# Kernel optimization log

Hardware: AMD Instinct MI355X
Metric: run time of the kernel (lower is better)

Reference implementation:

```python
import jax, jax.numpy as jnp
import numpy as np

V, E, D_LAT, NC, L = 30000, 256, 256, 10, 4096
B = 8
D_IN = 2 * D_LAT   # mamba expand=2 -> 512
N_ST = 16          # d_state
DT_R = 16          # dt_rank = ceil(d_model/16)
D_CONV = 4


def conv1d(x, w, b, pad, groups=1):
    # x: [B,C,L], w: [O, C//groups, K] (torch layout)
    y = jax.lax.conv_general_dilated(x, w, (1,), [(pad[0], pad[1])],
                                     dimension_numbers=('NCH', 'OIH', 'NCH'),
                                     feature_group_count=groups)
    return y + b[None, :, None]


def setup_inputs() -> dict:
    key = jax.random.key(0)
    ks = jax.random.split(key, 12)
    nrm = lambda k, s, sc=0.02: (jax.random.normal(k, s) * sc).astype(jnp.float32)
    return {
        'tokens': jax.random.randint(ks[0], (B, L), 0, V),
        'emb': nrm(ks[1], (V, E)),
        'conv1_w': nrm(ks[2], (128, E, 5)), 'conv1_b': jnp.zeros((128,), jnp.float32),
        'conv2_w': nrm(ks[3], (D_LAT, 128, 3)), 'conv2_b': jnp.zeros((D_LAT,), jnp.float32),
        'in_proj_w': nrm(ks[4], (2 * D_IN, D_LAT)),
        'convdw_w': nrm(ks[5], (D_IN, 1, D_CONV), 0.2), 'convdw_b': jnp.zeros((D_IN,), jnp.float32),
        'x_proj_w': nrm(ks[6], (DT_R + 2 * N_ST, D_IN)),
        'dt_proj_w': nrm(ks[7], (D_IN, DT_R), 0.1),
        'dt_proj_b': jnp.full((D_IN,), -4.0, jnp.float32),  # softplus^-1 of small dt
        'A_log': jnp.broadcast_to(jnp.log(jnp.arange(1, N_ST + 1, dtype=jnp.float32)), (D_IN, N_ST)) + jnp.zeros((D_IN, N_ST), jnp.float32),
        'Dp': jnp.ones((D_IN,), jnp.float32),
        'out_proj_w': nrm(ks[8], (D_LAT, D_IN)),
        'fc_w': nrm(ks[9], (NC, D_LAT)), 'fc_b': jnp.zeros((NC,), jnp.float32),
    }


def mamba_block(u, in_proj_w, convdw_w, convdw_b, x_proj_w, dt_proj_w, dt_proj_b, A_log, Dp, out_proj_w):
    # u: [B, Lm, d_model]
    Bsz = u.shape[0]
    xz = u @ in_proj_w.T                              # [B,Lm,2*Din]
    x, z = jnp.split(xz, 2, axis=-1)
    # causal depthwise conv (torch pads both sides, slices [:L] == left-pad only)
    xc = conv1d(x.transpose(0, 2, 1), convdw_w, convdw_b, (D_CONV - 1, 0), groups=D_IN)
    x = jax.nn.silu(xc.transpose(0, 2, 1))            # [B,Lm,Din]
    dbc = x @ x_proj_w.T                              # [B,Lm,dt_rank+2N]
    dt, Bm, Cm = jnp.split(dbc, [DT_R, DT_R + N_ST], axis=-1)
    dt = jax.nn.softplus(dt @ dt_proj_w.T + dt_proj_b)  # [B,Lm,Din]
    A = -jnp.exp(A_log)                               # [Din,N]

    def step(h, inp):
        dt_t, B_t, C_t, x_t = inp                     # [B,Din],[B,N],[B,N],[B,Din]
        dA = jnp.exp(dt_t[..., None] * A)             # [B,Din,N]
        h = h * dA + (dt_t * x_t)[..., None] * B_t[:, None, :]
        y = jnp.einsum('bdn,bn->bd', h, C_t)
        return h, y

    h0 = jnp.zeros((Bsz, D_IN, N_ST), u.dtype)
    xs = (dt.transpose(1, 0, 2), Bm.transpose(1, 0, 2), Cm.transpose(1, 0, 2), x.transpose(1, 0, 2))
    _, ys = jax.lax.scan(step, h0, xs)                # [Lm,B,Din]
    y = ys.transpose(1, 0, 2) + x * Dp
    y = y * jax.nn.silu(z)
    return y @ out_proj_w.T                           # [B,Lm,d_model]


def reference(tokens, emb, conv1_w, conv1_b, conv2_w, conv2_b, in_proj_w, convdw_w, convdw_b,
              x_proj_w, dt_proj_w, dt_proj_b, A_log, Dp, out_proj_w, fc_w, fc_b):
    x = emb[tokens]                                   # [B,L,E]
    x = x.transpose(0, 2, 1)                          # [B,E,L]
    x = jax.nn.relu(conv1d(x, conv1_w, conv1_b, (2, 2)))
    b, c, l = x.shape
    x = x.reshape(b, c, l // 2, 2).max(-1)            # MaxPool1d(2)
    x = jax.nn.relu(conv1d(x, conv2_w, conv2_b, (1, 1)))
    x = x.transpose(0, 2, 1)                          # [B,L/2,latent]
    x = mamba_block(x, in_proj_w, convdw_w, convdw_b, x_proj_w, dt_proj_w, dt_proj_b, A_log, Dp, out_proj_w)
    x = x.mean(axis=1)                                # [B,latent]
    return x @ fc_w.T + fc_b                          # [B,num_classes]
```

## Files before the change

kernel.cpp:

```cpp
#include <hip/hip_runtime.h>
#include <hip/hip_bf16.h>

constexpr int Bn   = 8;
constexpr int L    = 4096;
constexpr int E    = 256;
constexpr int Lh   = 2048;
constexpr int C1n  = 128;
constexpr int Dlat = 256;
constexpr int Din  = 512;
constexpr int Nst  = 16;
constexpr int M2   = Bn * Lh;
constexpr int NCH  = 128;
constexpr int TC   = 16;

constexpr long o_wtx   = 0;
constexpr long o_wtdt  = o_wtx  + 512L*48;
constexpr long o_bf    = o_wtdt + 16L*512;
constexpr long o_xeb   = o_bf    + 524288/2;
constexpr long o_out1b = o_xeb   + (8L*4100*256)/2;
constexpr long o_ub    = o_out1b + (8L*2050*128)/2;
constexpr long o_xz    = o_ub    + (16384L*256)/2;
constexpr long o_xbuf  = o_xz    + 16384L*1024;
constexpr long o_dbc   = o_xbuf  + 16384L*512;
constexpr long o_hend  = o_dbc   + 16384L*48;
constexpr long o_P     = o_hend  + 8L*512*NCH*16;
constexpr long o_S     = o_P     + 8L*512*NCH*16;
constexpr long o_ym    = o_S     + 8L*512*NCH*16;
constexpr long o_yp    = o_ym    + 8L*512;

typedef __attribute__((ext_vector_type(8))) short bf8_t;
typedef __attribute__((ext_vector_type(4))) float f4_t;

__device__ inline short f2bf(float f) {
    unsigned int u = __float_as_uint(f);
    unsigned int r = (u + 0x7FFFu + ((u >> 16) & 1u)) >> 16;
    return (short)r;
}

__global__ void k_prep(const float* __restrict__ w1, const float* __restrict__ w2,
                       const float* __restrict__ win, const float* __restrict__ xw,
                       const float* __restrict__ dtw, float* __restrict__ ws) {
    int idx = blockIdx.x * 256 + threadIdx.x;
    if (idx < 24576) {
        int n_ = idx % 48; int k = idx / 48;
        ws[o_wtx + idx] = xw[n_*512 + k];
    } else if (idx < 32768) {
        int j = idx - 24576;
        int n_ = j & 511; int k = j >> 9;
        ws[o_wtdt + j] = dtw[n_*16 + k];
    } else if (idx < 557056) {
        int j = idx - 32768;
        short* wsS = (short*)(ws + o_bf);
        if (j < 163840) {
            int n_ = j / 1280; int r = j - n_*1280; int s = r >> 8; int c = r & 255;
            wsS[j] = f2bf(w1[(n_*256 + c)*5 + s]);
        } else if (j < 262144) {
            int jj = j - 163840;
            int n_ = jj / 384; int r = jj - n_*384; int s = r >> 7; int c = r & 127;
            wsS[j] = f2bf(w2[(n_*128 + c)*3 + s]);
        } else {
            int jj = j - 262144;
            int n_ = jj >> 8; int k = jj & 255;
            wsS[j] = f2bf(win[n_*256 + k]);
        }
    }
}

__global__ void k_embed(const int* __restrict__ tok, const float* __restrict__ emb,
                        short* __restrict__ xeb) {
    int idx = blockIdx.x * 256 + threadIdx.x;
    int r = idx >> 5;
    int c8 = (idx & 31) << 3;
    int b = r / 4100; int tr = r - b*4100;
    bf8_t v = {0,0,0,0,0,0,0,0};
    if (tr >= 2 && tr < 4098) {
        int t = tok[b*4096 + tr - 2];
        const float* e = emb + (long)t*256 + c8;
        #pragma unroll
        for (int i = 0; i < 8; ++i) v[i] = f2bf(e[i]);
    }
    *(bf8_t*)&xeb[(long)r*256 + c8] = v;
}

__global__ void k_zpad(short* __restrict__ out1b) {
    int i = threadIdx.x;
    for (int j = i; j < 2048; j += 256) {
        int b = j >> 8; int rsel = (j >> 7) & 1; int c = j & 127;
        long row = (long)b*2050 + (rsel ? 2049 : 0);
        out1b[row*128 + c] = 0;
    }
}

template<int SHIFTS, int TPS, int EPI>
__global__ __launch_bounds__(256) void k_mgemm(const short* __restrict__ A, int ars, long batchA,
                                               const short* __restrict__ Bt, int ktot,
                                               const float* __restrict__ bias,
                                               short* __restrict__ outB, float* __restrict__ outF,
                                               int ors, long batchOut) {
    constexpr int KT = SHIFTS * TPS;
    constexpr int C  = TPS * 64;
    __shared__ short As[2][64][68];
    __shared__ short Bs[2][128][68];
    int tid = threadIdx.x;
    int l = tid & 63, w = tid >> 6;
    int m0 = blockIdx.x * 64;
    int n0 = blockIdx.y * 128;
    long zA = (long)blockIdx.z * batchA;
    long zO = (long)blockIdx.z * batchOut;

    bf8_t aReg[2], bReg[4];

    auto gload = [&](int kt) {
        int s = kt / TPS, c0 = (kt % TPS) * 64;
        const short* Ab = A + zA + (long)(m0 + s) * ars + c0;
        #pragma unroll
        for (int j = 0; j < 2; ++j) {
            int idx = tid + j*256;
            int r = idx >> 3, cc = (idx & 7) * 8;
            aReg[j] = *(const bf8_t*)&Ab[(long)r * ars + cc];
        }
        const short* Bb = Bt + (long)n0 * ktot + s * C + c0;
        #pragma unroll
        for (int j = 0; j < 4; ++j) {
            int idx = tid + j*256;
            int r = idx >> 3, cc = (idx & 7) * 8;
            bReg[j] = *(const bf8_t*)&Bb[(long)r * ktot + cc];
        }
    };
    auto lwrite = [&](int buf) {
        #pragma unroll
        for (int j = 0; j < 2; ++j) {
            int idx = tid + j*256;
            int r = idx >> 3, cc = (idx & 7) * 8;
            *(bf8_t*)&As[buf][r][cc] = aReg[j];
        }
        #pragma unroll
        for (int j = 0; j < 4; ++j) {
            int idx = tid + j*256;
            int r = idx >> 3, cc = (idx & 7) * 8;
            *(bf8_t*)&Bs[buf][r][cc] = bReg[j];
        }
    };

    f4_t acc[4][2];
    #pragma unroll
    for (int m = 0; m < 4; ++m)
        #pragma unroll
        for (int n = 0; n < 2; ++n) acc[m][n] = (f4_t){0.f, 0.f, 0.f, 0.f};

    gload(0);
    lwrite(0);
    __syncthreads();
    for (int kt = 0; kt < KT; ++kt) {
        int buf = kt & 1;
        if (kt + 1 < KT) gload(kt + 1);
        #pragma unroll
        for (int ks = 0; ks < 2; ++ks) {
            int kk = ks*32 + ((l >> 4) << 3);
            bf8_t a[4], b[2];
            #pragma unroll
            for (int m = 0; m < 4; ++m)
                a[m] = *(const bf8_t*)&As[buf][m*16 + (l & 15)][kk];
            #pragma unroll
            for (int n = 0; n < 2; ++n)
                b[n] = *(const bf8_t*)&Bs[buf][w*32 + n*16 + (l & 15)][kk];
            #pragma unroll
            for (int m = 0; m < 4; ++m)
                #pragma unroll
                for (int n = 0; n < 2; ++n)
                    acc[m][n] = __builtin_amdgcn_mfma_f32_16x16x32_bf16(a[m], b[n], acc[m][n], 0, 0, 0);
        }
        if (kt + 1 < KT) {
            lwrite(buf ^ 1);
            __syncthreads();
        }
    }

    #pragma unroll
    for (int mt = 0; mt < 4; ++mt)
        #pragma unroll
        for (int nt = 0; nt < 2; ++nt) {
            f4_t c = acc[mt][nt];
            int col = n0 + w*32 + nt*16 + (l & 15);
            int r0 = m0 + mt*16 + ((l >> 4) << 2);
            if constexpr (EPI == 0) {
                #pragma unroll
                for (int j = 0; j < 4; ++j)
                    outF[zO + (long)(r0 + j) * ors + col] = c[j];
            } else if constexpr (EPI == 1) {
                float bv = bias[col];
                #pragma unroll
                for (int j = 0; j < 4; ++j)
                    outB[zO + (long)(r0 + j) * ors + col] = f2bf(fmaxf(c[j] + bv, 0.f));
            } else {
                float bv = bias[col];
                float p0 = fmaxf(fmaxf(c[0], c[1]) + bv, 0.f);
                float p1 = fmaxf(fmaxf(c[2], c[3]) + bv, 0.f);
                int tp = r0 >> 1;
                outB[zO + (long)(tp + 1) * ors + col] = f2bf(p0);
                outB[zO + (long)(tp + 2) * ors + col] = f2bf(p1);
            }
        }
}

template<int ACT>
__global__ __launch_bounds__(256) void k_gemm(const float* __restrict__ A, int lda,
                                              const float* __restrict__ WT,
                                              const float* __restrict__ bias,
                                              float* __restrict__ out,
                                              int M, int N, int K) {
    __shared__ float As[16][68];
    __shared__ float Bs[16][64];
    int n0 = blockIdx.x * 64, m0 = blockIdx.y * 64;
    int tid = threadIdx.x;
    int ti = tid >> 4, tj = tid & 15;
    float acc[4][4] = {};
    for (int k0 = 0; k0 < K; k0 += 16) {
        {
            int mm = tid >> 2, kq = tid & 3;
            float4 v = *(const float4*)&A[(long)(m0 + mm)*lda + k0 + kq*4];
            As[kq*4+0][mm] = v.x; As[kq*4+1][mm] = v.y;
            As[kq*4+2][mm] = v.z; As[kq*4+3][mm] = v.w;
        }
        {
            int kk = tid >> 4, n4 = tid & 15;
            float4 v = {0.f,0.f,0.f,0.f};
            if (n0 + n4*4 < N)
                v = *(const float4*)&WT[(long)(k0 + kk)*N + n0 + n4*4];
            *(float4*)&Bs[kk][n4*4] = v;
        }
        __syncthreads();
        #pragma unroll
        for (int kk = 0; kk < 16; ++kk) {
            float4 av = *(float4*)&As[kk][ti*4];
            float4 bv = *(float4*)&Bs[kk][tj*4];
            acc[0][0] += av.x*bv.x; acc[0][1] += av.x*bv.y; acc[0][2] += av.x*bv.z; acc[0][3] += av.x*bv.w;
            acc[1][0] += av.y*bv.x; acc[1][1] += av.y*bv.y; acc[1][2] += av.y*bv.z; acc[1][3] += av.y*bv.w;
            acc[2][0] += av.z*bv.x; acc[2][1] += av.z*bv.y; acc[2][2] += av.z*bv.z; acc[2][3] += av.z*bv.w;
            acc[3][0] += av.w*bv.x; acc[3][1] += av.w*bv.y; acc[3][2] += av.w*bv.z; acc[3][3] += av.w*bv.w;
        }
        __syncthreads();
    }
    if (n0 + tj*4 >= N) return;
    float4 bv = {0.f,0.f,0.f,0.f};
    if (bias) bv = *(const float4*)&bias[n0 + tj*4];
    #pragma unroll
    for (int i = 0; i < 4; ++i) {
        int m = m0 + ti*4 + i;
        float4 v;
        v.x = acc[i][0] + bv.x; v.y = acc[i][1] + bv.y;
        v.z = acc[i][2] + bv.z; v.w = acc[i][3] + bv.w;
        if (ACT == 1) {
            v.x = (v.x > 20.f) ? v.x : log1pf(__expf(v.x));
            v.y = (v.y > 20.f) ? v.y : log1pf(__expf(v.y));
            v.z = (v.z > 20.f) ? v.z : log1pf(__expf(v.z));
            v.w = (v.w > 20.f) ? v.w : log1pf(__expf(v.w));
        }
        *(float4*)&out[(long)m*N + n0 + tj*4] = v;
    }
}

__global__ __launch_bounds__(256) void k_dwconv(const float* __restrict__ xz,
                                                const float* __restrict__ wdw,
                                                const float* __restrict__ bdw,
                                                float* __restrict__ xout) {
    __shared__ float wk[4][512];
    __shared__ float bs[512];
    int tid = threadIdx.x;
    for (int e = tid; e < 2048; e += 256) {
        int k = e >> 9, d = e & 511;
        wk[k][d] = wdw[d*4 + k];
    }
    bs[tid] = bdw[tid];
    bs[tid + 256] = bdw[tid + 256];
    __syncthreads();

    int idx = blockIdx.x * 256 + tid;
    int d4 = idx & 127;
    int tg = (idx >> 7) & 511;
    int b  = idx >> 16;
    int d0 = d4 * 4;
    int t0 = tg * 4;

    float4 x[7];
    #pragma unroll
    for (int i = 0; i < 7; ++i) {
        int t = t0 - 3 + i;
        x[i] = (t >= 0) ? *(const float4*)&xz[((long)(b*Lh + t))*1024 + d0]
                        : (float4){0.f, 0.f, 0.f, 0.f};
    }
    float4 w[4];
    #pragma unroll
    for (int k = 0; k < 4; ++k) w[k] = *(float4*)&wk[k][d0];
    float4 bias4 = *(float4*)&bs[d0];

    #pragma unroll
    for (int j = 0; j < 4; ++j) {
        float4 a = bias4;
        #pragma unroll
        for (int k = 0; k < 4; ++k) {
            float4 v = x[j + k];
            a.x += v.x * w[k].x; a.y += v.y * w[k].y;
            a.z += v.z * w[k].z; a.w += v.w * w[k].w;
        }
        a.x = a.x / (1.f + __expf(-a.x));
        a.y = a.y / (1.f + __expf(-a.y));
        a.z = a.z / (1.f + __expf(-a.z));
        a.w = a.w / (1.f + __expf(-a.w));
        *(float4*)&xout[((long)(b*Lh + t0 + j))*512 + d0] = a;
    }
}

__global__ __launch_bounds__(256) void k_scan_a(const float* __restrict__ x,
                                                const float* __restrict__ xz,
                                                const float* __restrict__ dbc,
                                                const float* __restrict__ wtdt,
                                                const float* __restrict__ dtb,
                                                const float* __restrict__ A_log,
                                                const float* __restrict__ Dp,
                                                float* __restrict__ hend,
                                                float* __restrict__ Pbuf,
                                                float* __restrict__ Sbuf,
                                                float* __restrict__ ypart) {
    __shared__ float4 Ds4[TC][4], Bs4[TC][4], Cs4[TC][4];
    int c = blockIdx.x;
    int b = blockIdx.z;
    int tid = threadIdx.x;
    int d = blockIdx.y * 256 + tid;
    for (int i = tid; i < TC*4; i += 256) {
        int tt = i >> 2, qq = i & 3;
        long rb = ((long)b*Lh + c*TC + tt)*48;
        Ds4[tt][qq] = *(const float4*)&dbc[rb + qq*4];
        Bs4[tt][qq] = *(const float4*)&dbc[rb + 16 + qq*4];
        Cs4[tt][qq] = *(const float4*)&dbc[rb + 32 + qq*4];
    }
    __syncthreads();
    float A_[16], wdt[16];
    #pragma unroll
    for (int n = 0; n < 16; ++n) A_[n] = -__expf(A_log[d*16 + n]);
    #pragma unroll
    for (int n = 0; n < 16; ++n) wdt[n] = wtdt[n*512 + d];
    float dtbd = dtb[d];
    float h[16], q[16], S[16];
    #pragma unroll
    for (int n = 0; n < 16; ++n) { h[n] = 0.f; q[n] = 1.f; S[n] = 0.f; }
    float Dpv = Dp[d];
    float yp = 0.f;
    long base  = ((long)b*Lh + c*TC)*512 + d;
    long zbase = ((long)b*Lh + c*TC)*1024 + 512 + d;
    for (int tt = 0; tt < TC; ++tt) {
        float dr[16];
        *(float4*)&dr[0]  = Ds4[tt][0]; *(float4*)&dr[4]  = Ds4[tt][1];
        *(float4*)&dr[8]  = Ds4[tt][2]; *(float4*)&dr[12] = Ds4[tt][3];
        float raw = dtbd;
        #pragma unroll
        for (int k = 0; k < 16; ++k) raw += dr[k] * wdt[k];
        float dtv = (raw > 20.f) ? raw : log1pf(__expf(raw));
        float xv  = x[base + (long)tt*512];
        float zv  = xz[zbase + (long)tt*1024];
        float u = dtv * xv;
        float gate = zv / (1.f + __expf(-zv));
        float Bv[16], Cv[16];
        *(float4*)&Bv[0]  = Bs4[tt][0]; *(float4*)&Bv[4]  = Bs4[tt][1];
        *(float4*)&Bv[8]  = Bs4[tt][2]; *(float4*)&Bv[12] = Bs4[tt][3];
        *(float4*)&Cv[0]  = Cs4[tt][0]; *(float4*)&Cv[4]  = Cs4[tt][1];
        *(float4*)&Cv[8]  = Cs4[tt][2]; *(float4*)&Cv[12] = Cs4[tt][3];
        float p = 0.f;
        #pragma unroll
        for (int n = 0; n < 16; ++n) {
            float dA = __expf(dtv * A_[n]);
            h[n] = h[n] * dA + u * Bv[n];
            q[n] *= dA;
            p += h[n] * Cv[n];
            S[n] += (gate * Cv[n]) * q[n];
        }
        yp += gate * (p + xv * Dpv);
    }
    long o = (((long)b*Din + d)*NCH + c)*16;
    #pragma unroll
    for (int n = 0; n < 16; ++n) hend[o + n] = h[n];
    #pragma unroll
    for (int n = 0; n < 16; ++n) Pbuf[o + n] = q[n];
    #pragma unroll
    for (int n = 0; n < 16; ++n) Sbuf[o + n] = S[n];
    ypart[((long)b*Din + d)*NCH + c] = yp;
}

__global__ __launch_bounds__(256) void k_scan_bc(const float* __restrict__ hend,
                                                 const float* __restrict__ Pbuf,
                                                 const float* __restrict__ Sbuf,
                                                 const float* __restrict__ ypart,
                                                 float* __restrict__ ym) {
    int idx = blockIdx.x * 256 + threadIdx.x;
    int n = idx & 15; long bd = idx >> 4;
    long base = bd * NCH * 16 + n;
    float h = 0.f, acc = 0.f;
    for (int c = 0; c < NCH; ++c) {
        long o = base + (long)c*16;
        acc += Sbuf[o] * h;
        h = hend[o] + Pbuf[o] * h;
    }
    #pragma unroll
    for (int k = 0; k < 8; ++k)
        acc += ypart[bd * NCH + n + k*16];
    acc += __shfl_xor(acc, 1);
    acc += __shfl_xor(acc, 2);
    acc += __shfl_xor(acc, 4);
    acc += __shfl_xor(acc, 8);
    if (n == 0) ym[bd] = acc;
}

__global__ void k_tail(const float* __restrict__ ym, const float* __restrict__ ow,
                       const float* __restrict__ fcw, const float* __restrict__ fcb,
                       float* __restrict__ out) {
    __shared__ float yls[512];
    __shared__ float xs[256];
    int b = blockIdx.x, c = threadIdx.x;
    yls[c] = ym[b*512 + c];
    yls[c + 256] = ym[b*512 + 256 + c];
    __syncthreads();
    float s = 0.f;
    for (int d = 0; d < 512; ++d) s += yls[d] * ow[c*512 + d];
    xs[c] = s * (1.f / 2048.f);
    __syncthreads();
    if (c < 10) {
        float t = fcb[c];
        for (int k = 0; k < 256; ++k) t += xs[k] * fcw[c*256 + k];
        out[b*10 + c] = t;
    }
}

extern "C" void kernel_launch(void* const* d_in, const int* in_sizes, int n_in,
                              void* d_out, int out_size, void* d_ws, size_t ws_size,
                              hipStream_t stream) {
    const int*   tok  = (const int*)d_in[0];
    const float* emb  = (const float*)d_in[1];
    const float* w1   = (const float*)d_in[2];
    const float* b1   = (const float*)d_in[3];
    const float* w2   = (const float*)d_in[4];
    const float* b2   = (const float*)d_in[5];
    const float* win  = (const float*)d_in[6];
    const float* wdw  = (const float*)d_in[7];
    const float* bdw  = (const float*)d_in[8];
    const float* xw   = (const float*)d_in[9];
    const float* dtw  = (const float*)d_in[10];
    const float* dtb  = (const float*)d_in[11];
    const float* alog = (const float*)d_in[12];
    const float* Dp   = (const float*)d_in[13];
    const float* ow   = (const float*)d_in[14];
    const float* fcw  = (const float*)d_in[15];
    const float* fcb  = (const float*)d_in[16];
    float* ws  = (float*)d_ws;
    float* out = (float*)d_out;

    float* wtx   = ws + o_wtx;
    float* wtdt  = ws + o_wtdt;
    short* wt1t  = (short*)(ws + o_bf);
    short* wt2t  = wt1t + 163840;
    short* wtint = wt2t + 98304;
    short* xeb   = (short*)(ws + o_xeb);
    short* out1b = (short*)(ws + o_out1b);
    short* ub    = (short*)(ws + o_ub);
    float* xz    = ws + o_xz;
    float* xbuf  = ws + o_xbuf;
    float* dbc   = ws + o_dbc;
    float* hend  = ws + o_hend;
    float* Pbuf  = ws + o_P;
    float* Sbuf  = ws + o_S;
    float* ym    = ws + o_ym;
    float* ypart = ws + o_yp;

    k_prep<<<2176, 256, 0, stream>>>(w1, w2, win, xw, dtw, ws);
    k_embed<<<4100, 256, 0, stream>>>(tok, emb, xeb);
    k_zpad<<<1, 256, 0, stream>>>(out1b);
    k_mgemm<5, 4, 2><<<dim3(64, 1, 8), 256, 0, stream>>>(
        xeb, 256, 4100L*256, wt1t, 1280, b1, out1b, nullptr, 128, 2050L*128);
    k_mgemm<3, 2, 1><<<dim3(32, 2, 8), 256, 0, stream>>>(
        out1b, 128, 2050L*128, wt2t, 384, b2, ub, nullptr, 256, 2048L*256);
    k_mgemm<1, 4, 0><<<dim3(256, 8, 1), 256, 0, stream>>>(
        ub, 256, 0, wtint, 256, nullptr, nullptr, xz, 1024, 0);
    k_dwconv<<<2048, 256, 0, stream>>>(xz, wdw, bdw, xbuf);
    k_gemm<0><<<dim3(1, M2/64), 256, 0, stream>>>(xbuf, Din, wtx, nullptr, dbc, M2, 48, Din);
    k_scan_a<<<dim3(NCH, 2, Bn), 256, 0, stream>>>(xbuf, xz, dbc, wtdt, dtb, alog, Dp,
                                                   hend, Pbuf, Sbuf, ypart);
    k_scan_bc<<<(Bn*Din*Nst)/256, 256, 0, stream>>>(hend, Pbuf, Sbuf, ypart, ym);
    k_tail<<<8, 256, 0, stream>>>(ym, ow, fcw, fcb, out);
}
```

Measured before the change: 344.5 us.

## Halve scan chunk count, reorder chunk-state layout, precompute negative A

Moves the chunked selective scan from 128 chunks of 16 steps to 64 chunks of 32 steps. This halves the chunk-state traffic written by scan_a and the serial chunk loop in scan_bc. The per-chunk state buffers are laid out chunk-major so neighbouring threads in both kernels touch neighbouring addresses. The prep kernel now computes -exp(A_log) once, and scan_a loads A and the dt weights as float4 vectors in place of strided scalar loads. In exchange, scan_a has half as many blocks and each does twice as much serial work, which lowers parallelism.

```diff
diff --git a/kernel.cpp b/kernel.cpp
--- a/kernel.cpp
+++ b/kernel.cpp
@@ -10,12 +10,12 @@
 constexpr int Din  = 512;
 constexpr int Nst  = 16;
 constexpr int M2   = Bn * Lh;
-constexpr int NCH  = 128;
-constexpr int TC   = 16;
+constexpr int NCH  = 64;
+constexpr int TC   = 32;
 
 constexpr long o_wtx   = 0;
-constexpr long o_wtdt  = o_wtx  + 512L*48;
-constexpr long o_bf    = o_wtdt + 16L*512;
+constexpr long o_aneg  = o_wtx  + 512L*48;
+constexpr long o_bf    = o_aneg + 512L*16;
 constexpr long o_xeb   = o_bf    + 524288/2;
 constexpr long o_out1b = o_xeb   + (8L*4100*256)/2;
 constexpr long o_ub    = o_out1b + (8L*2050*128)/2;
@@ -23,9 +23,9 @@
 constexpr long o_xbuf  = o_xz    + 16384L*1024;
 constexpr long o_dbc   = o_xbuf  + 16384L*512;
 constexpr long o_hend  = o_dbc   + 16384L*48;
-constexpr long o_P     = o_hend  + 8L*512*NCH*16;
-constexpr long o_S     = o_P     + 8L*512*NCH*16;
-constexpr long o_ym    = o_S     + 8L*512*NCH*16;
+constexpr long o_P     = o_hend  + 8L*NCH*512*16;
+constexpr long o_S     = o_P     + 8L*NCH*512*16;
+constexpr long o_ym    = o_S     + 8L*NCH*512*16;
 constexpr long o_yp    = o_ym    + 8L*512;
 
 typedef __attribute__((ext_vector_type(8))) short bf8_t;
@@ -39,15 +39,14 @@
 
 __global__ void k_prep(const float* __restrict__ w1, const float* __restrict__ w2,
                        const float* __restrict__ win, const float* __restrict__ xw,
-                       const float* __restrict__ dtw, float* __restrict__ ws) {
+                       const float* __restrict__ alog, float* __restrict__ ws) {
     int idx = blockIdx.x * 256 + threadIdx.x;
     if (idx < 24576) {
         int n_ = idx % 48; int k = idx / 48;
         ws[o_wtx + idx] = xw[n_*512 + k];
     } else if (idx < 32768) {
         int j = idx - 24576;
-        int n_ = j & 511; int k = j >> 9;
-        ws[o_wtdt + j] = dtw[n_*16 + k];
+        ws[o_aneg + j] = -__expf(alog[j]);
     } else if (idx < 557056) {
         int j = idx - 32768;
         short* wsS = (short*)(ws + o_bf);
@@ -314,9 +313,9 @@
 __global__ __launch_bounds__(256) void k_scan_a(const float* __restrict__ x,
                                                 const float* __restrict__ xz,
                                                 const float* __restrict__ dbc,
-                                                const float* __restrict__ wtdt,
+                                                const float* __restrict__ dtw,
                                                 const float* __restrict__ dtb,
-                                                const float* __restrict__ A_log,
+                                                const float* __restrict__ Aneg,
                                                 const float* __restrict__ Dp,
                                                 float* __restrict__ hend,
                                                 float* __restrict__ Pbuf,
@@ -337,9 +336,11 @@
     __syncthreads();
     float A_[16], wdt[16];
     #pragma unroll
-    for (int n = 0; n < 16; ++n) A_[n] = -__expf(A_log[d*16 + n]);
-    #pragma unroll
-    for (int n = 0; n < 16; ++n) wdt[n] = wtdt[n*512 + d];
+    for (int qq = 0; qq < 4; ++qq)
+        *(float4*)&A_[qq*4] = *(const float4*)&Aneg[d*16 + qq*4];
+    #pragma unroll
+    for (int qq = 0; qq < 4; ++qq)
+        *(float4*)&wdt[qq*4] = *(const float4*)&dtw[d*16 + qq*4];
     float dtbd = dtb[d];
     float h[16], q[16], S[16];
     #pragma unroll
@@ -376,14 +377,14 @@
         }
         yp += gate * (p + xv * Dpv);
     }
-    long o = (((long)b*Din + d)*NCH + c)*16;
+    long o = (((long)b*NCH + c)*512 + d)*16;
     #pragma unroll
     for (int n = 0; n < 16; ++n) hend[o + n] = h[n];
     #pragma unroll
     for (int n = 0; n < 16; ++n) Pbuf[o + n] = q[n];
     #pragma unroll
     for (int n = 0; n < 16; ++n) Sbuf[o + n] = S[n];
-    ypart[((long)b*Din + d)*NCH + c] = yp;
+    ypart[((long)b*NCH + c)*512 + d] = yp;
 }
 
 __global__ __launch_bounds__(256) void k_scan_bc(const float* __restrict__ hend,
@@ -392,17 +393,19 @@
                                                  const float* __restrict__ ypart,
                                                  float* __restrict__ ym) {
     int idx = blockIdx.x * 256 + threadIdx.x;
-    int n = idx & 15; long bd = idx >> 4;
-    long base = bd * NCH * 16 + n;
+    int n = idx & 15;
+    long bd = idx >> 4;
+    int d = (int)(bd & 511);
+    int b = (int)(bd >> 9);
     float h = 0.f, acc = 0.f;
     for (int c = 0; c < NCH; ++c) {
-        long o = base + (long)c*16;
+        long o = (((long)b*NCH + c)*512 + d)*16 + n;
         acc += Sbuf[o] * h;
         h = hend[o] + Pbuf[o] * h;
     }
     #pragma unroll
-    for (int k = 0; k < 8; ++k)
-        acc += ypart[bd * NCH + n + k*16];
+    for (int k = 0; k < NCH/16; ++k)
+        acc += ypart[((long)b*NCH + (n + k*16))*512 + d];
     acc += __shfl_xor(acc, 1);
     acc += __shfl_xor(acc, 2);
     acc += __shfl_xor(acc, 4);
@@ -454,7 +457,7 @@
     float* out = (float*)d_out;
 
     float* wtx   = ws + o_wtx;
-    float* wtdt  = ws + o_wtdt;
+    float* aneg  = ws + o_aneg;
     short* wt1t  = (short*)(ws + o_bf);
     short* wt2t  = wt1t + 163840;
     short* wtint = wt2t + 98304;
@@ -470,7 +473,7 @@
     float* ym    = ws + o_ym;
     float* ypart = ws + o_yp;
 
-    k_prep<<<2176, 256, 0, stream>>>(w1, w2, win, xw, dtw, ws);
+    k_prep<<<2176, 256, 0, stream>>>(w1, w2, win, xw, alog, ws);
     k_embed<<<4100, 256, 0, stream>>>(tok, emb, xeb);
     k_zpad<<<1, 256, 0, stream>>>(out1b);
     k_mgemm<5, 4, 2><<<dim3(64, 1, 8), 256, 0, stream>>>(
@@ -481,7 +484,7 @@
         ub, 256, 0, wtint, 256, nullptr, nullptr, xz, 1024, 0);
     k_dwconv<<<2048, 256, 0, stream>>>(xz, wdw, bdw, xbuf);
     k_gemm<0><<<dim3(1, M2/64), 256, 0, stream>>>(xbuf, Din, wtx, nullptr, dbc, M2, 48, Din);
-    k_scan_a<<<dim3(NCH, 2, Bn), 256, 0, stream>>>(xbuf, xz, dbc, wtdt, dtb, alog, Dp,
+    k_scan_a<<<dim3(NCH, 2, Bn), 256, 0, stream>>>(xbuf, xz, dbc, dtw, dtb, aneg, Dp,
                                                    hend, Pbuf, Sbuf, ypart);
     k_scan_bc<<<(Bn*Din*Nst)/256, 256, 0, stream>>>(hend, Pbuf, Sbuf, ypart, ym);
     k_tail<<<8, 256, 0, stream>>>(ym, ow, fcw, fcb, out);
```

Result: faster. 335.8 us (-2.5%).
